# Performance work log

Hardware: AMD Instinct MI355X
Metric: run time of the kernel (lower is better)

Reference implementation:

```python
import jax, jax.numpy as jnp
import numpy as np

B = 1 << 20
N_FREQS = 6          # sin+cos -> 3*2*6 = 36 dims for position
N_BINS = 4           # one-blob bins -> 4 dims per scalar
W_SCALE = 0.18       # ~ sqrt(2/64) He init for ReLU


def freq_embed(p):
    # p: [B,3] -> [B, 3*2*N_FREQS] NeRF-style sin/cos frequency encoding
    freqs = (2.0 ** jnp.arange(N_FREQS, dtype=p.dtype)) * jnp.pi  # [F]
    ang = p[:, :, None] * freqs  # [B,3,F]
    return jnp.concatenate([jnp.sin(ang), jnp.cos(ang)], axis=-1).reshape(p.shape[0], -1)


def one_blob_embed(x):
    # x: [B,D] values in [0,1] -> [B, D*N_BINS] Gaussian one-blob encoding
    centers = (jnp.arange(N_BINS, dtype=x.dtype) + 0.5) / N_BINS  # [K]
    sigma = 1.0 / N_BINS
    val = jnp.exp(-0.5 * ((x[:, :, None] - centers) / sigma) ** 2)  # [B,D,K]
    return val.reshape(x.shape[0], -1)


def to_sphe_coords(d):
    # unit direction [B,3] -> normalized (theta, phi) in [0,1]^2
    theta = jnp.arccos(jnp.clip(d[:, 2], -1.0, 1.0)) / jnp.pi
    phi = jnp.arctan2(d[:, 1], d[:, 0]) / (2.0 * jnp.pi) + 0.5
    return jnp.stack([theta, phi], axis=-1)


def setup_inputs() -> dict:
    key = jax.random.key(0)
    ks = jax.random.split(key, 13)
    p = jax.random.normal(ks[0], (B, 3), dtype=jnp.float32)
    wi = jax.random.normal(ks[1], (B, 3), dtype=jnp.float32)
    wi = wi / jnp.linalg.norm(wi, axis=-1, keepdims=True)
    n = jax.random.normal(ks[2], (B, 3), dtype=jnp.float32)
    n = n / jnp.linalg.norm(n, axis=-1, keepdims=True)
    alpha = jax.random.uniform(ks[3], (B, 3), dtype=jnp.float32)
    beta = jax.random.uniform(ks[4], (B, 3), dtype=jnp.float32)
    r = jax.random.uniform(ks[5], (B, 1), dtype=jnp.float32)
    Ws = {}
    for i in range(6):
        Ws[f"W{i}"] = jax.random.normal(ks[6 + i], (64, 64), dtype=jnp.float32) * W_SCALE
    Ws["W6"] = jax.random.normal(ks[12], (3, 64), dtype=jnp.float32) * W_SCALE
    return dict(p=p, wi=wi, n=n, alpha=alpha, beta=beta, r=r, **Ws)


def reference(p, wi, n, alpha, beta, r, W0, W1, W2, W3, W4, W5, W6):
    x = jnp.concatenate([
        freq_embed(p),                               # 36
        one_blob_embed(to_sphe_coords(wi)),          # 8
        one_blob_embed(to_sphe_coords(n)),           # 8
        one_blob_embed(1.0 - jnp.exp(-r)),           # 4
        alpha,                                       # 3
        beta,                                        # 3
        jnp.ones_like(p[:, :2]),                     # 2 (implicit bias)
    ], axis=-1)  # [B,64]
    h = x
    for W in (W0, W1, W2, W3, W4, W5):
        h = jax.nn.relu(h @ W.T)
    out = h @ W6.T  # [B,3]
    return out * (alpha + beta)  # reflectance factorization
```

## Files before the change

kernel.cpp:

```cpp
#include <hip/hip_runtime.h>

typedef __attribute__((ext_vector_type(8))) short short8;
typedef __attribute__((ext_vector_type(4))) float f32x4;

typedef __attribute__((address_space(3))) unsigned short lds_us;
typedef const __attribute__((address_space(1))) unsigned short glb_us;

__device__ __forceinline__ unsigned short f2bf(float x) {
  union { float f; unsigned u; } v; v.f = x;
  unsigned r = v.u + 0x7fffu + ((v.u >> 16) & 1u);
  return (unsigned short)(r >> 16);
}

#if __has_builtin(__builtin_amdgcn_cvt_pk_bf16_f32)
__device__ __forceinline__ unsigned pk2(float a, float b) {
  return __builtin_bit_cast(unsigned, __builtin_amdgcn_cvt_pk_bf16_f32(a, b));
}
#else
__device__ __forceinline__ unsigned pk2(float a, float b) {
  union { float f; unsigned u; } x, y; x.f = a; y.f = b;
  return __builtin_amdgcn_perm(y.u + 0x8000u, x.u + 0x8000u, 0x07060302u);
}
#endif

__device__ __forceinline__ unsigned relu_pk(unsigned x) {
  unsigned r;
  asm("v_pk_max_i16 %0, %1, %2" : "=v"(r) : "v"(x), "v"(0));
  return r;
}

__device__ __forceinline__ short8 u2s8(uint4 u) {
  union { uint4 a; short8 b; } c; c.a = u; return c.b;
}

__device__ __forceinline__ void wave_mem_fence() {
  asm volatile("" ::: "memory");
  __builtin_amdgcn_wave_barrier();
  asm volatile("" ::: "memory");
}

__device__ __forceinline__ void gload16(const unsigned short* g, unsigned short* l) {
  __builtin_amdgcn_global_load_lds((glb_us*)g, (lds_us*)l, 16, 0, 0);
}

__device__ __forceinline__ float acos01(float z) {
  float ax = fminf(fabsf(z), 1.0f);
  float t  = __builtin_amdgcn_sqrtf(1.0f - ax);
  float p  = fmaf(ax, fmaf(ax, fmaf(ax, -0.00596110f, 0.02363618f),
                           -0.06751692f), 0.49998766f);
  p *= t;
  return z >= 0.0f ? p : 1.0f - p;
}

__device__ __forceinline__ float atan2_01(float y, float x) {
  float ax = fabsf(x), ay = fabsf(y);
  float hi = fmaxf(ax, ay), lo = fminf(ax, ay);
  float r  = lo * __builtin_amdgcn_rcpf(fmaxf(hi, 1e-30f));
  float r2 = r * r;
  float p  = fmaf(r2, fmaf(r2, fmaf(r2, fmaf(r2, fmaf(r2,
               -0.0018655370f, 0.0083800422f), -0.018531250f),
                0.030803547f), -0.052940457f), 0.159151323f);
  float q  = r * p;
  q = (ay > ax) ? 0.25f - q : q;
  q = (x < 0.0f) ? 0.5f - q : q;
  return 0.5f + ((y >= 0.0f) ? q : -q);
}

__device__ __forceinline__ uint2 blob4pk(float x) {
  float x4 = x * 4.0f;
  float e0, e1, e2, e3;
  { float t = x4 - 0.5f; e0 = __builtin_amdgcn_exp2f(t * t * -0.72134752f); }
  { float t = x4 - 1.5f; e1 = __builtin_amdgcn_exp2f(t * t * -0.72134752f); }
  { float t = x4 - 2.5f; e2 = __builtin_amdgcn_exp2f(t * t * -0.72134752f); }
  { float t = x4 - 3.5f; e3 = __builtin_amdgcn_exp2f(t * t * -0.72134752f); }
  return make_uint2(pk2(e0, e1), pk2(e2, e3));
}

__device__ __forceinline__ void freq6(float p, float* s, float* c) {
  float fr = __builtin_amdgcn_fractf(0.5f * p);
  float sv = __builtin_amdgcn_sinf(fr);
  float cv = __builtin_amdgcn_cosf(fr);
  s[0] = sv; c[0] = cv;
#pragma unroll
  for (int i = 1; i < 6; ++i) {
    float t  = sv * cv;
    float ss = sv * sv;
    sv = t + t;
    cv = 1.0f - (ss + ss);
    s[i] = sv; c[i] = cv;
  }
}

__global__ void prep_weights(
    const float* __restrict__ W0, const float* __restrict__ W1,
    const float* __restrict__ W2, const float* __restrict__ W3,
    const float* __restrict__ W4, const float* __restrict__ W5,
    const float* __restrict__ W6, unsigned short* __restrict__ wb)
{
  int idx = blockIdx.x * blockDim.x + threadIdx.x;
  if (idx < 24576) {
    int l = idx >> 12;
    const float* W = (l==0)?W0:(l==1)?W1:(l==2)?W2:(l==3)?W3:(l==4)?W4:W5;
    int j   = idx & 7;
    int ln  = (idx >> 3) & 63;
    int h   = (idx >> 9) & 1;
    int t   = (idx >> 10) & 3;
    int n15 = ln & 15, q = ln >> 4;
    int src = 32*(t>>1) + 8*(n15>>2) + 4*(t&1) + (n15&3);
    int col = h*32 + q*8 + j;
    wb[idx] = f2bf(W[src*64 + col]);
  } else if (idx < 25600) {
    int i6  = idx - 24576;
    int j   = i6 & 7;
    int ln  = (i6 >> 3) & 63;
    int h   = (i6 >> 9) & 1;
    int n15 = ln & 15, q = ln >> 4;
    wb[idx] = (n15 < 3) ? f2bf(W6[n15*64 + h*32 + q*8 + j]) : (unsigned short)0;
  }
}

struct Enc {
  float p0,p1,p2, wx,wy,wz, nx,ny,nz, a0,a1,a2, e0,e1,e2, rr;
};

__device__ __forceinline__ Enc load_inputs(
    const float* __restrict__ P, const float* __restrict__ WI,
    const float* __restrict__ NRM, const float* __restrict__ ALPHA,
    const float* __restrict__ BETA, const float* __restrict__ R, int row)
{
  Enc v;
  v.p0 = P[row*3+0];  v.p1 = P[row*3+1];  v.p2 = P[row*3+2];
  v.wx = WI[row*3+0]; v.wy = WI[row*3+1]; v.wz = WI[row*3+2];
  v.nx = NRM[row*3+0]; v.ny = NRM[row*3+1]; v.nz = NRM[row*3+2];
  v.a0 = ALPHA[row*3+0]; v.a1 = ALPHA[row*3+1]; v.a2 = ALPHA[row*3+2];
  v.e0 = BETA[row*3+0];  v.e1 = BETA[row*3+1];  v.e2 = BETA[row*3+2];
  v.rr = R[row];
  return v;
}

__device__ __forceinline__ void encode_stage(
    const Enc& v, unsigned short* __restrict__ Xw,
    int lane, int n15, int q, uint4* b0, uint4* b1)
{
  unsigned short* xr = Xw + lane*40;

  float s0[6], c0[6], s1[6], c1[6], s2[6], c2[6];
  freq6(v.p0, s0, c0);
  freq6(v.p1, s1, c1);
  freq6(v.p2, s2, c2);

  *(uint4*)(xr +  0) = make_uint4(pk2(s0[0],s0[1]), pk2(s0[2],s0[3]),
                                  pk2(s0[4],s0[5]), pk2(c0[0],c0[1]));
  *(uint4*)(xr +  8) = make_uint4(pk2(c0[2],c0[3]), pk2(c0[4],c0[5]),
                                  pk2(s1[0],s1[1]), pk2(s1[2],s1[3]));
  *(uint4*)(xr + 16) = make_uint4(pk2(s1[4],s1[5]), pk2(c1[0],c1[1]),
                                  pk2(c1[2],c1[3]), pk2(c1[4],c1[5]));
  *(uint4*)(xr + 24) = make_uint4(pk2(s2[0],s2[1]), pk2(s2[2],s2[3]),
                                  pk2(s2[4],s2[5]), pk2(c2[0],c2[1]));
  wave_mem_fence();
#pragma unroll
  for (int g = 0; g < 4; ++g)
    b0[g] = *(const uint4*)(Xw + (g*16 + n15)*40 + q*8);
  wave_mem_fence();

  uint2 bwt = blob4pk(acos01(v.wz));
  uint2 bwp = blob4pk(atan2_01(v.wy, v.wx));
  uint2 bnt = blob4pk(acos01(v.nz));
  uint2 bnp = blob4pk(atan2_01(v.ny, v.nx));
  uint2 brr = blob4pk(1.0f - __builtin_amdgcn_exp2f(v.rr * -1.44269504f));

  *(uint4*)(xr +  0) = make_uint4(pk2(c2[2],c2[3]), pk2(c2[4],c2[5]),
                                  bwt.x, bwt.y);
  *(uint4*)(xr +  8) = make_uint4(bwp.x, bwp.y, bnt.x, bnt.y);
  *(uint4*)(xr + 16) = make_uint4(bnp.x, bnp.y, brr.x, brr.y);
  *(uint4*)(xr + 24) = make_uint4(pk2(v.a0,v.a1), pk2(v.a2,v.e0),
                                  pk2(v.e1,v.e2), 0x3F803F80u);
  wave_mem_fence();
#pragma unroll
  for (int g = 0; g < 4; ++g)
    b1[g] = *(const uint4*)(Xw + (g*16 + n15)*40 + q*8);
  wave_mem_fence();
}

__global__ __launch_bounds__(256, 2) void nrc_mlp(
    const float* __restrict__ P, const float* __restrict__ WI,
    const float* __restrict__ NRM, const float* __restrict__ ALPHA,
    const float* __restrict__ BETA, const float* __restrict__ R,
    const unsigned short* __restrict__ wb, float* __restrict__ out)
{
  __shared__ __align__(16) unsigned short lds[35840];
  const int lane = threadIdx.x & 63;
  const int wv   = threadIdx.x >> 6;
  const int n15  = lane & 15;
  const int q    = lane >> 4;
  const int l16  = lane * 8;
  unsigned short* Xw = lds + 25600 + wv*2560;
  const int blkrow = blockIdx.x * 2048;

  Enc iv = load_inputs(P, WI, NRM, ALPHA, BETA, R, blkrow + wv*64 + lane);

  for (int c = wv; c < 50; c += 4)
    gload16(wb + c*512 + l16, lds + c*512 + l16);

  uint4 b0[4], b1[4];
  encode_stage(iv, Xw, lane, n15, q, b0, b1);

  __syncthreads();

  const f32x4 z = {0.f, 0.f, 0.f, 0.f};

#pragma unroll 1
  for (int t = 0; t < 8; ++t) {
    Enc ivn;
    if (t < 7)
      ivn = load_inputs(P, WI, NRM, ALPHA, BETA, R,
                        blkrow + (t+1)*256 + wv*64 + lane);

#pragma unroll
    for (int l = 0; l < 6; ++l) {
      const unsigned short* Wl = lds + l*4096;
      short8 a0[4], a1[4];
#pragma unroll
      for (int k = 0; k < 4; ++k) {
        a0[k] = *(const short8*)(Wl + k*1024 + l16);
        a1[k] = *(const short8*)(Wl + k*1024 + 512 + l16);
      }
      f32x4 acc[4][4];
#pragma unroll
      for (int k = 0; k < 4; ++k) {
#pragma unroll
        for (int g = 0; g < 4; ++g) {
          f32x4 c = __builtin_amdgcn_mfma_f32_16x16x32_bf16(a0[k], u2s8(b0[g]), z, 0, 0, 0);
          acc[g][k] = __builtin_amdgcn_mfma_f32_16x16x32_bf16(a1[k], u2s8(b1[g]), c, 0, 0, 0);
        }
      }
#pragma unroll
      for (int g = 0; g < 4; ++g) {
        uint4 n0, n1;
        n0.x = relu_pk(pk2(acc[g][0][0], acc[g][0][1]));
        n0.y = relu_pk(pk2(acc[g][0][2], acc[g][0][3]));
        n0.z = relu_pk(pk2(acc[g][1][0], acc[g][1][1]));
        n0.w = relu_pk(pk2(acc[g][1][2], acc[g][1][3]));
        n1.x = relu_pk(pk2(acc[g][2][0], acc[g][2][1]));
        n1.y = relu_pk(pk2(acc[g][2][2], acc[g][2][3]));
        n1.z = relu_pk(pk2(acc[g][3][0], acc[g][3][1]));
        n1.w = relu_pk(pk2(acc[g][3][2], acc[g][3][3]));
        b0[g] = n0; b1[g] = n1;
      }
    }

    {
      const unsigned short* W6l = lds + 24576;
      short8 o0 = *(const short8*)(W6l + l16);
      short8 o1 = *(const short8*)(W6l + 512 + l16);
      const int row0 = blkrow + t*256 + wv*64;
#pragma unroll
      for (int g = 0; g < 4; ++g) {
        f32x4 c = __builtin_amdgcn_mfma_f32_16x16x32_bf16(o0, u2s8(b0[g]), z, 0, 0, 0);
        c       = __builtin_amdgcn_mfma_f32_16x16x32_bf16(o1, u2s8(b1[g]), c, 0, 0, 0);
        if (q == 0) {
          int base = row0*3 + g*48 + n15*3;
          float3 av = *(const float3*)(ALPHA + base);
          float3 bv = *(const float3*)(BETA + base);
          float3 o;
          o.x = c[0] * (av.x + bv.x);
          o.y = c[1] * (av.y + bv.y);
          o.z = c[2] * (av.z + bv.z);
          *(float3*)(out + base) = o;
        }
      }
    }

    if (t < 7)
      encode_stage(ivn, Xw, lane, n15, q, b0, b1);
  }
}

extern "C" void kernel_launch(void* const* d_in, const int* in_sizes, int n_in,
                              void* d_out, int out_size, void* d_ws, size_t ws_size,
                              hipStream_t stream) {
  const float* P  = (const float*)d_in[0];
  const float* WI = (const float*)d_in[1];
  const float* NR = (const float*)d_in[2];
  const float* AL = (const float*)d_in[3];
  const float* BE = (const float*)d_in[4];
  const float* R  = (const float*)d_in[5];
  const float* W0 = (const float*)d_in[6];
  const float* W1 = (const float*)d_in[7];
  const float* W2 = (const float*)d_in[8];
  const float* W3 = (const float*)d_in[9];
  const float* W4 = (const float*)d_in[10];
  const float* W5 = (const float*)d_in[11];
  const float* W6 = (const float*)d_in[12];
  unsigned short* wb = (unsigned short*)d_ws;
  float* out = (float*)d_out;

  prep_weights<<<100, 256, 0, stream>>>(W0, W1, W2, W3, W4, W5, W6, wb);
  nrc_mlp<<<512, 256, 0, stream>>>(P, WI, NR, AL, BE, R, wb, out);
}
```

Baseline: 166.4 us.

## Stream weights per layer through double-buffered LDS, one tile per block

Each block now handles a single 256-row tile instead of looping over eight, with 4096 blocks launched. Weights are streamed per layer into a two-slot LDS buffer with a block barrier after each layer, so LDS drops from about 70KB to 32KB and launch bounds rise to 5 blocks per CU. The encode scratch now uses an XOR-swizzled 32-element row stride in place of 40-element padding to avoid bank conflicts. The trade is that every block reloads all weights from global/L2, pays six barriers per tile, and loses the software prefetch of the next tile's inputs.

```diff
diff --git a/kernel.cpp b/kernel.cpp
--- a/kernel.cpp
+++ b/kernel.cpp
@@ -142,25 +142,28 @@
     const Enc& v, unsigned short* __restrict__ Xw,
     int lane, int n15, int q, uint4* b0, uint4* b1)
 {
-  unsigned short* xr = Xw + lane*40;
+  unsigned short* xr = Xw + lane*32;
+  const int sw  = lane & 3;
+  const int swr = n15 & 3;
+#define XST(c) (*(uint4*)(xr + (((c) ^ sw) << 3)))
 
   float s0[6], c0[6], s1[6], c1[6], s2[6], c2[6];
   freq6(v.p0, s0, c0);
   freq6(v.p1, s1, c1);
   freq6(v.p2, s2, c2);
 
-  *(uint4*)(xr +  0) = make_uint4(pk2(s0[0],s0[1]), pk2(s0[2],s0[3]),
-                                  pk2(s0[4],s0[5]), pk2(c0[0],c0[1]));
-  *(uint4*)(xr +  8) = make_uint4(pk2(c0[2],c0[3]), pk2(c0[4],c0[5]),
-                                  pk2(s1[0],s1[1]), pk2(s1[2],s1[3]));
-  *(uint4*)(xr + 16) = make_uint4(pk2(s1[4],s1[5]), pk2(c1[0],c1[1]),
-                                  pk2(c1[2],c1[3]), pk2(c1[4],c1[5]));
-  *(uint4*)(xr + 24) = make_uint4(pk2(s2[0],s2[1]), pk2(s2[2],s2[3]),
-                                  pk2(s2[4],s2[5]), pk2(c2[0],c2[1]));
+  XST(0) = make_uint4(pk2(s0[0],s0[1]), pk2(s0[2],s0[3]),
+                      pk2(s0[4],s0[5]), pk2(c0[0],c0[1]));
+  XST(1) = make_uint4(pk2(c0[2],c0[3]), pk2(c0[4],c0[5]),
+                      pk2(s1[0],s1[1]), pk2(s1[2],s1[3]));
+  XST(2) = make_uint4(pk2(s1[4],s1[5]), pk2(c1[0],c1[1]),
+                      pk2(c1[2],c1[3]), pk2(c1[4],c1[5]));
+  XST(3) = make_uint4(pk2(s2[0],s2[1]), pk2(s2[2],s2[3]),
+                      pk2(s2[4],s2[5]), pk2(c2[0],c2[1]));
   wave_mem_fence();
 #pragma unroll
   for (int g = 0; g < 4; ++g)
-    b0[g] = *(const uint4*)(Xw + (g*16 + n15)*40 + q*8);
+    b0[g] = *(const uint4*)(Xw + (g*16 + n15)*32 + ((q ^ swr) << 3));
   wave_mem_fence();
 
   uint2 bwt = blob4pk(acos01(v.wz));
@@ -169,38 +172,41 @@
   uint2 bnp = blob4pk(atan2_01(v.ny, v.nx));
   uint2 brr = blob4pk(1.0f - __builtin_amdgcn_exp2f(v.rr * -1.44269504f));
 
-  *(uint4*)(xr +  0) = make_uint4(pk2(c2[2],c2[3]), pk2(c2[4],c2[5]),
-                                  bwt.x, bwt.y);
-  *(uint4*)(xr +  8) = make_uint4(bwp.x, bwp.y, bnt.x, bnt.y);
-  *(uint4*)(xr + 16) = make_uint4(bnp.x, bnp.y, brr.x, brr.y);
-  *(uint4*)(xr + 24) = make_uint4(pk2(v.a0,v.a1), pk2(v.a2,v.e0),
-                                  pk2(v.e1,v.e2), 0x3F803F80u);
+  XST(0) = make_uint4(pk2(c2[2],c2[3]), pk2(c2[4],c2[5]), bwt.x, bwt.y);
+  XST(1) = make_uint4(bwp.x, bwp.y, bnt.x, bnt.y);
+  XST(2) = make_uint4(bnp.x, bnp.y, brr.x, brr.y);
+  XST(3) = make_uint4(pk2(v.a0,v.a1), pk2(v.a2,v.e0),
+                      pk2(v.e1,v.e2), 0x3F803F80u);
   wave_mem_fence();
 #pragma unroll
   for (int g = 0; g < 4; ++g)
-    b1[g] = *(const uint4*)(Xw + (g*16 + n15)*40 + q*8);
+    b1[g] = *(const uint4*)(Xw + (g*16 + n15)*32 + ((q ^ swr) << 3));
   wave_mem_fence();
-}
-
-__global__ __launch_bounds__(256, 2) void nrc_mlp(
+#undef XST
+}
+
+__global__ __launch_bounds__(256, 5) void nrc_mlp(
     const float* __restrict__ P, const float* __restrict__ WI,
     const float* __restrict__ NRM, const float* __restrict__ ALPHA,
     const float* __restrict__ BETA, const float* __restrict__ R,
     const unsigned short* __restrict__ wb, float* __restrict__ out)
 {
-  __shared__ __align__(16) unsigned short lds[35840];
+  __shared__ __align__(16) unsigned short lds[16384];
   const int lane = threadIdx.x & 63;
   const int wv   = threadIdx.x >> 6;
   const int n15  = lane & 15;
   const int q    = lane >> 4;
   const int l16  = lane * 8;
-  unsigned short* Xw = lds + 25600 + wv*2560;
-  const int blkrow = blockIdx.x * 2048;
-
-  Enc iv = load_inputs(P, WI, NRM, ALPHA, BETA, R, blkrow + wv*64 + lane);
-
-  for (int c = wv; c < 50; c += 4)
-    gload16(wb + c*512 + l16, lds + c*512 + l16);
+  unsigned short* Xw = lds + 8192 + wv*2048;
+  const int row0 = (blockIdx.x * 4 + wv) * 64;
+
+  Enc iv = load_inputs(P, WI, NRM, ALPHA, BETA, R, row0 + lane);
+
+  {
+    int c0 = 2*wv*512;
+    gload16(wb + c0 + l16,        lds + c0 + l16);
+    gload16(wb + c0 + 512 + l16,  lds + c0 + 512 + l16);
+  }
 
   uint4 b0[4], b1[4];
   encode_stage(iv, Xw, lane, n15, q, b0, b1);
@@ -209,70 +215,71 @@
 
   const f32x4 z = {0.f, 0.f, 0.f, 0.f};
 
-#pragma unroll 1
-  for (int t = 0; t < 8; ++t) {
-    Enc ivn;
-    if (t < 7)
-      ivn = load_inputs(P, WI, NRM, ALPHA, BETA, R,
-                        blkrow + (t+1)*256 + wv*64 + lane);
-
-#pragma unroll
-    for (int l = 0; l < 6; ++l) {
-      const unsigned short* Wl = lds + l*4096;
-      short8 a0[4], a1[4];
-#pragma unroll
-      for (int k = 0; k < 4; ++k) {
-        a0[k] = *(const short8*)(Wl + k*1024 + l16);
-        a1[k] = *(const short8*)(Wl + k*1024 + 512 + l16);
+#pragma unroll
+  for (int l = 0; l < 6; ++l) {
+    if (l < 5) {
+      unsigned short* nb = lds + ((l+1) & 1) * 4096;
+      int ns = (l+1) * 4096;
+      int c0 = 2*wv*512;
+      gload16(wb + ns + c0 + l16,       nb + c0 + l16);
+      gload16(wb + ns + c0 + 512 + l16, nb + c0 + 512 + l16);
+    } else if (wv < 2) {
+      int c0 = wv*512;
+      gload16(wb + 24576 + c0 + l16, lds + c0 + l16);
+    }
+
+    const unsigned short* Wl = lds + (l & 1) * 4096;
+    short8 a0[4], a1[4];
+#pragma unroll
+    for (int k = 0; k < 4; ++k) {
+      a0[k] = *(const short8*)(Wl + k*1024 + l16);
+      a1[k] = *(const short8*)(Wl + k*1024 + 512 + l16);
+    }
+
+    f32x4 acc[4][4];
+#pragma unroll
+    for (int k = 0; k < 4; ++k) {
+#pragma unroll
+      for (int g = 0; g < 4; ++g) {
+        f32x4 c = __builtin_amdgcn_mfma_f32_16x16x32_bf16(a0[k], u2s8(b0[g]), z, 0, 0, 0);
+        acc[g][k] = __builtin_amdgcn_mfma_f32_16x16x32_bf16(a1[k], u2s8(b1[g]), c, 0, 0, 0);
       }
-      f32x4 acc[4][4];
-#pragma unroll
-      for (int k = 0; k < 4; ++k) {
-#pragma unroll
-        for (int g = 0; g < 4; ++g) {
-          f32x4 c = __builtin_amdgcn_mfma_f32_16x16x32_bf16(a0[k], u2s8(b0[g]), z, 0, 0, 0);
-          acc[g][k] = __builtin_amdgcn_mfma_f32_16x16x32_bf16(a1[k], u2s8(b1[g]), c, 0, 0, 0);
-        }
+    }
+
+#pragma unroll
+    for (int g = 0; g < 4; ++g) {
+      uint4 n0, n1;
+      n0.x = relu_pk(pk2(acc[g][0][0], acc[g][0][1]));
+      n0.y = relu_pk(pk2(acc[g][0][2], acc[g][0][3]));
+      n0.z = relu_pk(pk2(acc[g][1][0], acc[g][1][1]));
+      n0.w = relu_pk(pk2(acc[g][1][2], acc[g][1][3]));
+      n1.x = relu_pk(pk2(acc[g][2][0], acc[g][2][1]));
+      n1.y = relu_pk(pk2(acc[g][2][2], acc[g][2][3]));
+      n1.z = relu_pk(pk2(acc[g][3][0], acc[g][3][1]));
+      n1.w = relu_pk(pk2(acc[g][3][2], acc[g][3][3]));
+      b0[g] = n0; b1[g] = n1;
+    }
+    __syncthreads();
+  }
+
+  {
+    short8 o0 = *(const short8*)(lds + l16);
+    short8 o1 = *(const short8*)(lds + 512 + l16);
+#pragma unroll
+    for (int g = 0; g < 4; ++g) {
+      f32x4 c = __builtin_amdgcn_mfma_f32_16x16x32_bf16(o0, u2s8(b0[g]), z, 0, 0, 0);
+      c       = __builtin_amdgcn_mfma_f32_16x16x32_bf16(o1, u2s8(b1[g]), c, 0, 0, 0);
+      if (q == 0) {
+        int base = row0*3 + g*48 + n15*3;
+        float3 av = *(const float3*)(ALPHA + base);
+        float3 bv = *(const float3*)(BETA + base);
+        float3 o;
+        o.x = c[0] * (av.x + bv.x);
+        o.y = c[1] * (av.y + bv.y);
+        o.z = c[2] * (av.z + bv.z);
+        *(float3*)(out + base) = o;
       }
-#pragma unroll
-      for (int g = 0; g < 4; ++g) {
-        uint4 n0, n1;
-        n0.x = relu_pk(pk2(acc[g][0][0], acc[g][0][1]));
-        n0.y = relu_pk(pk2(acc[g][0][2], acc[g][0][3]));
-        n0.z = relu_pk(pk2(acc[g][1][0], acc[g][1][1]));
-        n0.w = relu_pk(pk2(acc[g][1][2], acc[g][1][3]));
-        n1.x = relu_pk(pk2(acc[g][2][0], acc[g][2][1]));
-        n1.y = relu_pk(pk2(acc[g][2][2], acc[g][2][3]));
-        n1.z = relu_pk(pk2(acc[g][3][0], acc[g][3][1]));
-        n1.w = relu_pk(pk2(acc[g][3][2], acc[g][3][3]));
-        b0[g] = n0; b1[g] = n1;
-      }
-    }
-
-    {
-      const unsigned short* W6l = lds + 24576;
-      short8 o0 = *(const short8*)(W6l + l16);
-      short8 o1 = *(const short8*)(W6l + 512 + l16);
-      const int row0 = blkrow + t*256 + wv*64;
-#pragma unroll
-      for (int g = 0; g < 4; ++g) {
-        f32x4 c = __builtin_amdgcn_mfma_f32_16x16x32_bf16(o0, u2s8(b0[g]), z, 0, 0, 0);
-        c       = __builtin_amdgcn_mfma_f32_16x16x32_bf16(o1, u2s8(b1[g]), c, 0, 0, 0);
-        if (q == 0) {
-          int base = row0*3 + g*48 + n15*3;
-          float3 av = *(const float3*)(ALPHA + base);
-          float3 bv = *(const float3*)(BETA + base);
-          float3 o;
-          o.x = c[0] * (av.x + bv.x);
-          o.y = c[1] * (av.y + bv.y);
-          o.z = c[2] * (av.z + bv.z);
-          *(float3*)(out + base) = o;
-        }
-      }
-    }
-
-    if (t < 7)
-      encode_stage(ivn, Xw, lane, n15, q, b0, b1);
+    }
   }
 }
 
@@ -296,5 +303,5 @@
   float* out = (float*)d_out;
 
   prep_weights<<<100, 256, 0, stream>>>(W0, W1, W2, W3, W4, W5, W6, wb);
-  nrc_mlp<<<512, 256, 0, stream>>>(P, WI, NR, AL, BE, R, wb, out);
-}
+  nrc_mlp<<<4096, 256, 0, stream>>>(P, WI, NR, AL, BE, R, wb, out);
+}
```

After: 168.6 us. About the same (+1.3%).
